# Kernel optimization log

Measured on AMD Instinct MI355X. Metric: run time of the kernel, lower is better.

## Reference

```python
import jax, jax.numpy as jnp
import numpy as np

# Tap patterns inside the 3x3 window (ky, kx) for each kernel_type.
# kernel_type=0 'skel' (5 taps): cross (center + 4-neighborhood).
SKEL_TAPS = [(0, 1), (1, 0), (1, 1), (1, 2), (2, 1)]


def build_dense_kernel(weight, taps):
    # weight: [O, C, K] sparse-tap weights -> dense [K*O, C, 3, 3] conv kernel,
    # kernel-major channel layout (j*O + o) to match torch.cat over tap dim.
    O, C, K = weight.shape
    dense = jnp.zeros((K, O, C, 3, 3), dtype=weight.dtype)
    for j, (ky, kx) in enumerate(taps):  # K is small and fixed (5)
        dense = dense.at[j, :, :, ky, kx].set(weight[:, :, j])
    return dense.reshape(K * O, C, 3, 3)


def setup_inputs() -> dict:
    key = jax.random.key(0)
    k1, k2 = jax.random.split(key)
    x = jax.random.normal(k1, (32, 128, 64, 64), dtype=jnp.float32)
    weight = jax.random.normal(k2, (128, 128, 5), dtype=jnp.float32) * 0.05
    return {"x": x, "weight": weight}


def reference(x, weight):
    # _SConv forward: sparse-tap conv producing [K, N, O, H, W]; spatial=True
    # concatenates the K per-tap slices along channels -> [N, K*O, H, W].
    # Expressed as a single dense 3x3 conv with zeros at non-tap positions.
    kernel = build_dense_kernel(weight, SKEL_TAPS)  # [K*O, C, 3, 3]
    out = jax.lax.conv_general_dilated(
        x, kernel,
        window_strides=(1, 1),
        padding=((1, 1), (1, 1)),
        rhs_dilation=(1, 1),
        dimension_numbers=("NCHW", "OIHW", "NCHW"),
    )  # [N, K*O, H, W]
    return jax.nn.relu(out)
```

## Files before the change

kernel.cpp:

```cpp
#include <hip/hip_runtime.h>
#include <hip/hip_bf16.h>

typedef __attribute__((ext_vector_type(8))) short bf16x8;
typedef __attribute__((ext_vector_type(4))) float f32x4;

__device__ __forceinline__ short f2bf(float v) {
    unsigned u = __builtin_bit_cast(unsigned, v);
    u += 0x7fffu + ((u >> 16) & 1u);
    return (short)(u >> 16);
}
__device__ __forceinline__ float relu(float v) { return v > 0.f ? v : 0.f; }

#define ROWP 68
#define CHP  136

__global__ __launch_bounds__(64)
void prep_wfrag(const float* __restrict__ w, bf16x8* __restrict__ wf) {
    const int mt   = blockIdx.x >> 2;
    const int kt   = blockIdx.x & 3;
    const int lane = threadIdx.x;
    const int j  = mt >> 3;
    const int ot = mt & 7;
    const int o  = ot * 16 + (lane & 15);
    const int c0 = kt * 32 + (lane >> 4) * 8;
    const float* wp = w + ((size_t)o * 128 + c0) * 5 + j;
    bf16x8 f;
    #pragma unroll
    for (int e = 0; e < 8; ++e) f[e] = f2bf(wp[e * 5]);
    wf[(size_t)(mt * 4 + kt) * 64 + lane] = f;
}

__global__ __launch_bounds__(512, 8)
void sconv_v8(const float* __restrict__ x, const bf16x8* __restrict__ wf,
              float* __restrict__ out) {
    __shared__ float lds[64 * CHP];

    const int bid = blockIdx.x;
    const int hp = bid & 31;
    const int n  = bid >> 5;
    const int h0 = hp * 2;

    const int t    = threadIdx.x;
    const int wave = t >> 6;
    const int lane = t & 63;
    const int l15  = lane & 15;
    const int lg   = lane >> 4;
    const int r    = wave >> 2;
    const int pt   = wave & 3;
    const int pos  = pt * 16 + l15;
    const int h    = h0 + r;

    const float* xb = x + (size_t)n * 128 * 4096 + (size_t)(h * 64 + pos);
    bf16x8 xf[4];
    #pragma unroll
    for (int kt = 0; kt < 4; ++kt) {
        const float* xp = xb + (size_t)(kt * 32 + lg * 8) * 4096;
        bf16x8 f;
        #pragma unroll
        for (int e = 0; e < 8; ++e) f[e] = f2bf(xp[(size_t)e * 4096]);
        xf[kt] = f;
    }

    const int wq  = pt * 4 + lg;
    const int wc0 = pt * 16 + lg * 4;

    #pragma unroll
    for (int j = 0; j < 5; ++j) {
        #pragma unroll
        for (int p = 0; p < 2; ++p) {
            if (j == 1 && t < 128)
                lds[(t >> 1) * CHP + (t & 1) * ROWP + 0] = 0.f;
            if (j == 3 && t < 128)
                lds[(t >> 1) * CHP + (t & 1) * ROWP + 63] = 0.f;

            #pragma unroll
            for (int oi = 0; oi < 4; ++oi) {
                const int ot = p * 4 + oi;
                const int cl = oi * 16 + l15;
                const bf16x8* wfp = wf + (size_t)((j * 8 + ot) * 4) * 64 + lane;
                f32x4 acc = {0.f, 0.f, 0.f, 0.f};
                #pragma unroll
                for (int kt = 0; kt < 4; ++kt)
                    acc = __builtin_amdgcn_mfma_f32_16x16x32_bf16(
                        xf[kt], wfp[(size_t)kt * 64], acc, 0, 0, 0);

                if (j == 0 || j == 2 || j == 4) {
                    f32x4 v;
                    #pragma unroll
                    for (int q = 0; q < 4; ++q) v[q] = relu(acc[q]);
                    *reinterpret_cast<f32x4*>(
                        &lds[cl * CHP + r * ROWP + wq * 4]) = v;
                } else {
                    #pragma unroll
                    for (int q = 0; q < 4; ++q) {
                        const int ws = wc0 + q + (j == 1 ? 1 : -1);
                        if ((unsigned)ws < 64u)
                            lds[cl * CHP + r * ROWP + ws] = relu(acc[q]);
                    }
                }
            }
            __syncthreads();

            #pragma unroll
            for (int i = 0; i < 4; ++i) {
                const int g  = i * 512 + t;
                const int cl = g >> 5;
                const int hr = (g >> 4) & 1;
                const int q  = g & 15;
                f32x4 v = *reinterpret_cast<const f32x4*>(
                    &lds[cl * CHP + hr * ROWP + q * 4]);
                const int hh = h0 + hr;
                const int hs = (j == 0) ? ((hh + 1) & 63)
                             : (j == 4) ? ((hh + 63) & 63) : hh;
                if ((j == 0 && hh == 63) || (j == 4 && hh == 0))
                    v = f32x4{0.f, 0.f, 0.f, 0.f};
                __builtin_nontemporal_store(
                    v, reinterpret_cast<f32x4*>(
                           out + (((size_t)n * 640 + j * 128 + p * 64 + cl) * 64
                                  + hs) * 64 + q * 4));
            }
            if (j < 4 || p < 1) __syncthreads();
        }
    }
}

__global__ __launch_bounds__(512, 2)
void sconv_mfma(const float* __restrict__ x, const float* __restrict__ w,
                float* __restrict__ out) {
    __shared__ bf16x8 wfrag[8][4][64];
    const int bid = blockIdx.x;
    const int j   = bid % 5;
    const int hp  = (bid / 5) % 32;
    const int n   = bid / 160;
    const int t = threadIdx.x;
    for (int s = t; s < 2048; s += 512) {
        const int lane = s & 63;
        const int rest = s >> 6;
        const int mt   = rest >> 2;
        const int kt   = rest & 3;
        const int o    = mt * 16 + (lane & 15);
        const int c0   = kt * 32 + (lane >> 4) * 8;
        const float* wp = w + ((size_t)o * 128 + c0) * 5 + j;
        bf16x8 f;
        #pragma unroll
        for (int e = 0; e < 8; ++e) f[e] = f2bf(wp[e * 5]);
        wfrag[mt][kt][lane] = f;
    }
    __syncthreads();
    const int wave = t >> 6;
    const int lane = t & 63;
    const int l15  = lane & 15;
    const int lg   = lane >> 4;
    const int h    = hp * 2 + (wave >> 2);
    const int wcol = (wave & 3) * 16 + l15;
    const int dy[5] = {-1, 0, 0, 0, 1};
    const int dx[5] = { 0,-1, 0, 1, 0};
    const int hi = h + dy[j];
    const int wi = wcol + dx[j];
    const bool valid = ((unsigned)hi < 64u) && ((unsigned)wi < 64u);
    const int hic = hi < 0 ? 0 : (hi > 63 ? 63 : hi);
    const int wic = wi < 0 ? 0 : (wi > 63 ? 63 : wi);
    const float* xb = x + (size_t)n * 128 * 4096 + (size_t)(hic * 64 + wic);
    bf16x8 xf[4];
    #pragma unroll
    for (int kt = 0; kt < 4; ++kt) {
        const int c0 = kt * 32 + lg * 8;
        const float* xp = xb + (size_t)c0 * 4096;
        bf16x8 f;
        #pragma unroll
        for (int e = 0; e < 8; ++e) {
            float v = xp[(size_t)e * 4096];
            f[e] = f2bf(valid ? v : 0.0f);
        }
        xf[kt] = f;
    }
    f32x4 acc[8];
    #pragma unroll
    for (int mt = 0; mt < 8; ++mt) acc[mt] = f32x4{0.f, 0.f, 0.f, 0.f};
    #pragma unroll
    for (int kt = 0; kt < 4; ++kt)
        #pragma unroll
        for (int mt = 0; mt < 8; ++mt)
            acc[mt] = __builtin_amdgcn_mfma_f32_16x16x32_bf16(
                wfrag[mt][kt][lane], xf[kt], acc[mt], 0, 0, 0);
    float* ob = out + ((size_t)n * 640 + (size_t)j * 128) * 4096
                    + (size_t)(h * 64 + wcol);
    #pragma unroll
    for (int mt = 0; mt < 8; ++mt) {
        const int ch = mt * 16 + lg * 4;
        #pragma unroll
        for (int r = 0; r < 4; ++r) {
            float v = acc[mt][r];
            ob[(size_t)(ch + r) * 4096] = v > 0.f ? v : 0.f;
        }
    }
}

extern "C" void kernel_launch(void* const* d_in, const int* in_sizes, int n_in,
                              void* d_out, int out_size, void* d_ws, size_t ws_size,
                              hipStream_t stream) {
    const float* x = (const float*)d_in[0];
    const float* w = (const float*)d_in[1];
    float* out = (float*)d_out;

    const size_t wf_bytes = (size_t)40 * 4 * 64 * sizeof(bf16x8);
    if (ws_size >= wf_bytes) {
        bf16x8* wf = (bf16x8*)d_ws;
        hipLaunchKernelGGL(prep_wfrag, dim3(160), dim3(64), 0, stream, w, wf);
        hipLaunchKernelGGL(sconv_v8, dim3(32 * 32), dim3(512), 0, stream,
                           x, wf, out);
    } else {
        hipLaunchKernelGGL(sconv_mfma, dim3(32 * 32 * 5), dim3(512), 0, stream,
                           x, w, out);
    }
}
```

Measured before the change: 80.19 us.

## Process four rows per block with two MFMA tiles per wave sharing weight loads

Each block now covers four output rows instead of two, and each wave computes two 16-pixel tiles that reuse the same weight fragment per MFMA step. This halves the global weight-fragment loads per output pixel and halves the grid size. The LDS staging buffer doubles to about 68 KB, which lowers achievable occupancy. The grid of 512 blocks may also underfill the GPU's compute units.

```diff
diff --git a/kernel.cpp b/kernel.cpp
--- a/kernel.cpp
+++ b/kernel.cpp
@@ -11,8 +11,8 @@
 }
 __device__ __forceinline__ float relu(float v) { return v > 0.f ? v : 0.f; }
 
-#define ROWP 68
-#define CHP  136
+#define ROWW 68
+#define CHW  272
 
 __global__ __launch_bounds__(64)
 void prep_wfrag(const float* __restrict__ w, bf16x8* __restrict__ wf) {
@@ -30,86 +30,91 @@
     wf[(size_t)(mt * 4 + kt) * 64 + lane] = f;
 }
 
-__global__ __launch_bounds__(512, 8)
-void sconv_v8(const float* __restrict__ x, const bf16x8* __restrict__ wf,
+__global__ __launch_bounds__(512, 4)
+void sconv_v9(const float* __restrict__ x, const bf16x8* __restrict__ wf,
               float* __restrict__ out) {
-    __shared__ float lds[64 * CHP];
+    __shared__ float lds[64 * CHW];
 
     const int bid = blockIdx.x;
-    const int hp = bid & 31;
-    const int n  = bid >> 5;
-    const int h0 = hp * 2;
+    const int hq = bid & 15;
+    const int n  = bid >> 4;
+    const int h0 = hq * 4;
 
     const int t    = threadIdx.x;
     const int wave = t >> 6;
     const int lane = t & 63;
     const int l15  = lane & 15;
     const int lg   = lane >> 4;
-    const int r    = wave >> 2;
-    const int pt   = wave & 3;
-    const int pos  = pt * 16 + l15;
+    const int r    = wave >> 1;
+    const int ph   = wave & 1;
     const int h    = h0 + r;
 
-    const float* xb = x + (size_t)n * 128 * 4096 + (size_t)(h * 64 + pos);
-    bf16x8 xf[4];
-    #pragma unroll
-    for (int kt = 0; kt < 4; ++kt) {
-        const float* xp = xb + (size_t)(kt * 32 + lg * 8) * 4096;
-        bf16x8 f;
-        #pragma unroll
-        for (int e = 0; e < 8; ++e) f[e] = f2bf(xp[(size_t)e * 4096]);
-        xf[kt] = f;
-    }
-
-    const int wq  = pt * 4 + lg;
-    const int wc0 = pt * 16 + lg * 4;
+    const float* xb = x + (size_t)n * 128 * 4096 + (size_t)(h * 64 + ph * 32 + l15);
+    bf16x8 xf[2][4];
+    #pragma unroll
+    for (int ta = 0; ta < 2; ++ta) {
+        #pragma unroll
+        for (int kt = 0; kt < 4; ++kt) {
+            const float* xp = xb + ta * 16 + (size_t)(kt * 32 + lg * 8) * 4096;
+            bf16x8 f;
+            #pragma unroll
+            for (int e = 0; e < 8; ++e) f[e] = f2bf(xp[(size_t)e * 4096]);
+            xf[ta][kt] = f;
+        }
+    }
+
+    const int qA  = ph * 8 + lg;
+    const int wcA = ph * 32 + lg * 4;
 
     #pragma unroll
     for (int j = 0; j < 5; ++j) {
         #pragma unroll
         for (int p = 0; p < 2; ++p) {
-            if (j == 1 && t < 128)
-                lds[(t >> 1) * CHP + (t & 1) * ROWP + 0] = 0.f;
-            if (j == 3 && t < 128)
-                lds[(t >> 1) * CHP + (t & 1) * ROWP + 63] = 0.f;
+            if (j == 1 && t < 256) lds[(t >> 2) * CHW + (t & 3) * ROWW + 0] = 0.f;
+            if (j == 3 && t < 256) lds[(t >> 2) * CHW + (t & 3) * ROWW + 63] = 0.f;
 
             #pragma unroll
             for (int oi = 0; oi < 4; ++oi) {
                 const int ot = p * 4 + oi;
                 const int cl = oi * 16 + l15;
                 const bf16x8* wfp = wf + (size_t)((j * 8 + ot) * 4) * 64 + lane;
-                f32x4 acc = {0.f, 0.f, 0.f, 0.f};
+                f32x4 a0 = {0.f, 0.f, 0.f, 0.f};
+                f32x4 a1 = {0.f, 0.f, 0.f, 0.f};
                 #pragma unroll
-                for (int kt = 0; kt < 4; ++kt)
-                    acc = __builtin_amdgcn_mfma_f32_16x16x32_bf16(
-                        xf[kt], wfp[(size_t)kt * 64], acc, 0, 0, 0);
-
+                for (int kt = 0; kt < 4; ++kt) {
+                    const bf16x8 b = wfp[(size_t)kt * 64];
+                    a0 = __builtin_amdgcn_mfma_f32_16x16x32_bf16(xf[0][kt], b, a0, 0, 0, 0);
+                    a1 = __builtin_amdgcn_mfma_f32_16x16x32_bf16(xf[1][kt], b, a1, 0, 0, 0);
+                }
+
+                float* const row = &lds[cl * CHW + r * ROWW];
                 if (j == 0 || j == 2 || j == 4) {
-                    f32x4 v;
+                    f32x4 v0, v1;
                     #pragma unroll
-                    for (int q = 0; q < 4; ++q) v[q] = relu(acc[q]);
-                    *reinterpret_cast<f32x4*>(
-                        &lds[cl * CHP + r * ROWP + wq * 4]) = v;
+                    for (int q = 0; q < 4; ++q) { v0[q] = relu(a0[q]); v1[q] = relu(a1[q]); }
+                    *reinterpret_cast<f32x4*>(row + qA * 4)       = v0;
+                    *reinterpret_cast<f32x4*>(row + (qA + 4) * 4) = v1;
                 } else {
+                    const int d = (j == 1) ? 1 : -1;
                     #pragma unroll
                     for (int q = 0; q < 4; ++q) {
-                        const int ws = wc0 + q + (j == 1 ? 1 : -1);
-                        if ((unsigned)ws < 64u)
-                            lds[cl * CHP + r * ROWP + ws] = relu(acc[q]);
+                        const int w0 = wcA + q + d;
+                        const int w1 = wcA + 16 + q + d;
+                        if ((unsigned)w0 < 64u) row[w0] = relu(a0[q]);
+                        if ((unsigned)w1 < 64u) row[w1] = relu(a1[q]);
                     }
                 }
             }
             __syncthreads();
 
             #pragma unroll
-            for (int i = 0; i < 4; ++i) {
-                const int g  = i * 512 + t;
-                const int cl = g >> 5;
-                const int hr = (g >> 4) & 1;
-                const int q  = g & 15;
+            for (int i = 0; i < 8; ++i) {
+                const int cl = i * 8 + wave;
+                const int rr = lane >> 4;
+                const int q  = lane & 15;
                 f32x4 v = *reinterpret_cast<const f32x4*>(
-                    &lds[cl * CHP + hr * ROWP + q * 4]);
-                const int hh = h0 + hr;
+                    &lds[cl * CHW + rr * ROWW + q * 4]);
+                const int hh = h0 + rr;
                 const int hs = (j == 0) ? ((hh + 1) & 63)
                              : (j == 4) ? ((hh + 63) & 63) : hh;
                 if ((j == 0 && hh == 63) || (j == 4 && hh == 0))
@@ -207,7 +212,7 @@
     if (ws_size >= wf_bytes) {
         bf16x8* wf = (bf16x8*)d_ws;
         hipLaunchKernelGGL(prep_wfrag, dim3(160), dim3(64), 0, stream, w, wf);
-        hipLaunchKernelGGL(sconv_v8, dim3(32 * 32), dim3(512), 0, stream,
+        hipLaunchKernelGGL(sconv_v9, dim3(32 * 16), dim3(512), 0, stream,
                            x, wf, out);
     } else {
         hipLaunchKernelGGL(sconv_mfma, dim3(32 * 32 * 5), dim3(512), 0, stream,
```

New measurement: 85.08 us. 1.06x slower.

## Split output-channel halves across wave groups, reusing each weight fragment for both rows

Applied to the files above, without the earlier changes.

Each wave now loads the input fragments for both spatial rows and computes only the half of the output channels (p) matching its wave group. Every weight fragment load then feeds two MFMAs, one per row, which halves per-wave weight traffic. The cost is twice the input-fragment registers per wave, and only half the waves issue MFMAs in each p phase, which may leave compute idle between barriers.

```diff
diff --git a/kernel.cpp b/kernel.cpp
--- a/kernel.cpp
+++ b/kernel.cpp
@@ -31,8 +31,8 @@
 }
 
 __global__ __launch_bounds__(512, 8)
-void sconv_v8(const float* __restrict__ x, const bf16x8* __restrict__ wf,
-              float* __restrict__ out) {
+void sconv_v11(const float* __restrict__ x, const bf16x8* __restrict__ wf,
+               float* __restrict__ out) {
     __shared__ float lds[64 * CHP];
 
     const int bid = blockIdx.x;
@@ -43,26 +43,29 @@
     const int t    = threadIdx.x;
     const int wave = t >> 6;
     const int lane = t & 63;
+    const int mh   = wave >> 2;
+    const int pt   = wave & 3;
     const int l15  = lane & 15;
     const int lg   = lane >> 4;
-    const int r    = wave >> 2;
-    const int pt   = wave & 3;
     const int pos  = pt * 16 + l15;
-    const int h    = h0 + r;
-
-    const float* xb = x + (size_t)n * 128 * 4096 + (size_t)(h * 64 + pos);
-    bf16x8 xf[4];
-    #pragma unroll
-    for (int kt = 0; kt < 4; ++kt) {
-        const float* xp = xb + (size_t)(kt * 32 + lg * 8) * 4096;
-        bf16x8 f;
-        #pragma unroll
-        for (int e = 0; e < 8; ++e) f[e] = f2bf(xp[(size_t)e * 4096]);
-        xf[kt] = f;
+
+    const float* xb = x + (size_t)n * 128 * 4096 + (size_t)(h0 * 64 + pos);
+    bf16x8 xf[2][4];
+    #pragma unroll
+    for (int r = 0; r < 2; ++r) {
+        #pragma unroll
+        for (int kt = 0; kt < 4; ++kt) {
+            const float* xp = xb + (size_t)r * 64
+                            + (size_t)(kt * 32 + lg * 8) * 4096;
+            bf16x8 f;
+            #pragma unroll
+            for (int e = 0; e < 8; ++e) f[e] = f2bf(xp[(size_t)e * 4096]);
+            xf[r][kt] = f;
+        }
     }
 
     const int wq  = pt * 4 + lg;
-    const int wc0 = pt * 16 + lg * 4;
+    const int wp0 = pt * 16 + lg * 4;
 
     #pragma unroll
     for (int j = 0; j < 5; ++j) {
@@ -73,29 +76,42 @@
             if (j == 3 && t < 128)
                 lds[(t >> 1) * CHP + (t & 1) * ROWP + 63] = 0.f;
 
-            #pragma unroll
-            for (int oi = 0; oi < 4; ++oi) {
-                const int ot = p * 4 + oi;
-                const int cl = oi * 16 + l15;
-                const bf16x8* wfp = wf + (size_t)((j * 8 + ot) * 4) * 64 + lane;
-                f32x4 acc = {0.f, 0.f, 0.f, 0.f};
+            if (mh == p) {
                 #pragma unroll
-                for (int kt = 0; kt < 4; ++kt)
-                    acc = __builtin_amdgcn_mfma_f32_16x16x32_bf16(
-                        xf[kt], wfp[(size_t)kt * 64], acc, 0, 0, 0);
-
-                if (j == 0 || j == 2 || j == 4) {
-                    f32x4 v;
+                for (int oi = 0; oi < 4; ++oi) {
+                    const int ot = p * 4 + oi;
+                    const int cl = oi * 16 + l15;
+                    const bf16x8* wfp =
+                        wf + (size_t)((j * 8 + ot) * 4) * 64 + lane;
+                    f32x4 a0 = {0.f, 0.f, 0.f, 0.f};
+                    f32x4 a1 = {0.f, 0.f, 0.f, 0.f};
                     #pragma unroll
-                    for (int q = 0; q < 4; ++q) v[q] = relu(acc[q]);
-                    *reinterpret_cast<f32x4*>(
-                        &lds[cl * CHP + r * ROWP + wq * 4]) = v;
-                } else {
-                    #pragma unroll
-                    for (int q = 0; q < 4; ++q) {
-                        const int ws = wc0 + q + (j == 1 ? 1 : -1);
-                        if ((unsigned)ws < 64u)
-                            lds[cl * CHP + r * ROWP + ws] = relu(acc[q]);
+                    for (int kt = 0; kt < 4; ++kt) {
+                        const bf16x8 b = wfp[(size_t)kt * 64];
+                        a0 = __builtin_amdgcn_mfma_f32_16x16x32_bf16(
+                            xf[0][kt], b, a0, 0, 0, 0);
+                        a1 = __builtin_amdgcn_mfma_f32_16x16x32_bf16(
+                            xf[1][kt], b, a1, 0, 0, 0);
+                    }
+                    float* const row0 = &lds[cl * CHP];
+                    if (j == 0 || j == 2 || j == 4) {
+                        f32x4 v0, v1;
+                        #pragma unroll
+                        for (int q = 0; q < 4; ++q) {
+                            v0[q] = relu(a0[q]); v1[q] = relu(a1[q]);
+                        }
+                        *reinterpret_cast<f32x4*>(row0 + wq * 4)        = v0;
+                        *reinterpret_cast<f32x4*>(row0 + ROWP + wq * 4) = v1;
+                    } else {
+                        const int d = (j == 1) ? 1 : -1;
+                        #pragma unroll
+                        for (int q = 0; q < 4; ++q) {
+                            const int ws = wp0 + q + d;
+                            if ((unsigned)ws < 64u) {
+                                row0[ws]        = relu(a0[q]);
+                                row0[ROWP + ws] = relu(a1[q]);
+                            }
+                        }
                     }
                 }
             }
@@ -207,7 +223,7 @@
     if (ws_size >= wf_bytes) {
         bf16x8* wf = (bf16x8*)d_ws;
         hipLaunchKernelGGL(prep_wfrag, dim3(160), dim3(64), 0, stream, w, wf);
-        hipLaunchKernelGGL(sconv_v8, dim3(32 * 32), dim3(512), 0, stream,
+        hipLaunchKernelGGL(sconv_v11, dim3(32 * 32), dim3(512), 0, stream,
                            x, wf, out);
     } else {
         hipLaunchKernelGGL(sconv_mfma, dim3(32 * 32 * 5), dim3(512), 0, stream,
```

Measured after the change: 82.44 us. 1.03x slower.
